# Performance work log

Measured on AMD Instinct MI355X. Metric: run time of the kernel, lower is better.

The kernel has to match this reference:

```python
import jax, jax.numpy as jnp
import numpy as np

D = 1024            # text/user embedding length
HID = 3 * D         # 2*text_D + user_D = MLP hidden width
OUT = 8             # output_shape (int)


def setup_inputs() -> dict:
    key = jax.random.key(0)
    ks = jax.random.split(key, 9)
    T, U = 256, 128
    s = 1.0 / np.sqrt(HID)
    return {
        "text_a": jax.random.normal(ks[0], (T, D), jnp.float32),
        "text_b": jax.random.normal(ks[1], (T, D), jnp.float32),
        "user_embeddings": jax.random.normal(ks[2], (U, D), jnp.float32),
        "W1": jax.random.uniform(ks[3], (HID, HID), jnp.float32, -s, s),
        "b1": jax.random.uniform(ks[4], (HID,), jnp.float32, -s, s),
        "W2": jax.random.uniform(ks[5], (HID, HID), jnp.float32, -s, s),
        "b2": jax.random.uniform(ks[6], (HID,), jnp.float32, -s, s),
        "W3": jax.random.uniform(ks[7], (OUT, HID), jnp.float32, -s, s),
        "b3": jax.random.uniform(ks[8], (OUT,), jnp.float32, -s, s),
    }


def reference(text_a, text_b, user_embeddings, W1, b1, W2, b2, W3, b3):
    # min/max over the set of text embedding tensors
    t_min = jnp.minimum(text_a, text_b)          # (T, D)
    t_max = jnp.maximum(text_a, text_b)          # (T, D)
    T, U = t_min.shape[0], user_embeddings.shape[0]
    # combined[t, u] = concat(t_min[t], t_max[t], user[u])  -> (T, U, 3D)
    text_part = jnp.broadcast_to(
        jnp.concatenate([t_min, t_max], axis=-1)[:, None, :], (T, U, 2 * D))
    user_part = jnp.broadcast_to(user_embeddings[None, :, :], (T, U, D))
    x = jnp.concatenate([text_part, user_part], axis=-1)  # (T, U, 3D)
    # 3-layer MLP (no activation, no dropout by default)
    x = jnp.einsum('tuh,oh->tuo', x, W1) + b1
    x = jnp.einsum('tuh,oh->tuo', x, W2) + b2
    x = jnp.einsum('tuh,oh->tuo', x, W3) + b3
    return x  # (T, U, OUT)
```

## Files before the change

### kernel.cpp

```cpp
#include <hip/hip_runtime.h>
#include <hip/hip_bf16.h>


#define HIDN 3072
#define DIM 1024
#define NOUT 8
#define NS 32
#define KPS 96
#define WK 24
#define GX 12
#define TDIM 256
#define UDIM 128

__device__ __forceinline__ float dot4(float4 a, float4 b) {
    return a.x * b.x + a.y * b.y + a.z * b.z + a.w * b.w;
}

__device__ __forceinline__ void bias_slice_fold(const float* As,
                                                const float* __restrict__ bvec,
                                                float* __restrict__ cp,
                                                int s, int tid) {
    const int o = tid >> 5, k5 = tid & 31;
    float acc = 0.f;
#pragma unroll
    for (int j = 0; j < KPS / 32; ++j)
        acc += As[o * KPS + k5 + 32 * j] * bvec[s * KPS + k5 + 32 * j];
#pragma unroll
    for (int off = 16; off; off >>= 1) acc += __shfl_down(acc, off, 32);
    if (k5 == 0) cp[s * NOUT + o] = acc;
}

__global__ __launch_bounds__(256) void gemm_partial(
    const float* __restrict__ A_rows, const float* __restrict__ part_in,
    const float* __restrict__ B, float* __restrict__ part_out,
    const float* __restrict__ bvec, float* __restrict__ cp, int mode) {
    const int s = blockIdx.y, gx = blockIdx.x;
    const int tid = threadIdx.x;
    const int lane = tid & 63, w = tid >> 6;

    __shared__ float As[NOUT * KPS];
    __shared__ float4 red[4 * NOUT * 64];

    if (mode == 0) {
        for (int i = tid; i < NOUT * KPS; i += 256)
            As[i] = A_rows[(i / KPS) * HIDN + s * KPS + (i % KPS)];
    } else {
        for (int j4 = tid; j4 < NOUT * KPS / 4; j4 += 256) {
            const int o = j4 / (KPS / 4), kk4 = j4 % (KPS / 4);
            const float4* pp = (const float4*)(part_in + (size_t)o * HIDN
                                               + s * KPS) + kk4;
            float4 a = make_float4(0.f, 0.f, 0.f, 0.f);
#pragma unroll 8
            for (int sp = 0; sp < NS; ++sp) {
                float4 v = pp[(size_t)sp * (NOUT * HIDN / 4)];
                a.x += v.x; a.y += v.y; a.z += v.z; a.w += v.w;
            }
            ((float4*)As)[j4] = a;
        }
    }
    __syncthreads();
    if (gx == 0) bias_slice_fold(As, bvec, cp, s, tid);

    const int h = gx * 256 + lane * 4;
    const int k0 = s * KPS + w * WK;
    const float4* Bp = (const float4*)(B + (size_t)k0 * HIDN) + (h >> 2);

    float4 bv[WK];
#pragma unroll
    for (int kk = 0; kk < WK; ++kk) bv[kk] = Bp[(size_t)kk * (HIDN / 4)];

    float4 acc[NOUT];
#pragma unroll
    for (int o = 0; o < NOUT; ++o) acc[o] = make_float4(0.f, 0.f, 0.f, 0.f);
#pragma unroll
    for (int kk = 0; kk < WK; ++kk) {
#pragma unroll
        for (int o = 0; o < NOUT; ++o) {
            float a = As[o * KPS + w * WK + kk];
            acc[o].x += a * bv[kk].x; acc[o].y += a * bv[kk].y;
            acc[o].z += a * bv[kk].z; acc[o].w += a * bv[kk].w;
        }
    }

#pragma unroll
    for (int o = 0; o < NOUT; ++o) red[(w * NOUT + o) * 64 + lane] = acc[o];
    __syncthreads();
#pragma unroll
    for (int j = 0; j < 2; ++j) {
        const int o = w * 2 + j;
        float4 v0 = red[(0 * NOUT + o) * 64 + lane];
        float4 v1 = red[(1 * NOUT + o) * 64 + lane];
        float4 v2 = red[(2 * NOUT + o) * 64 + lane];
        float4 v3 = red[(3 * NOUT + o) * 64 + lane];
        *(float4*)(part_out + ((size_t)s * NOUT + o) * HIDN + h) =
            make_float4(v0.x + v1.x + v2.x + v3.x, v0.y + v1.y + v2.y + v3.y,
                        v0.z + v1.z + v2.z + v3.z, v0.w + v1.w + v2.w + v3.w);
    }
}

__global__ __launch_bounds__(256) void reduce_M_c(const float* __restrict__ part,
                                                  const float* __restrict__ cp1,
                                                  const float* __restrict__ cp2,
                                                  const float* __restrict__ b3,
                                                  float* __restrict__ M,
                                                  float* __restrict__ c) {
    const int b = blockIdx.x, tid = threadIdx.x;
    if (b == 96) {
        if (tid < NOUT) {
            float acc = b3[tid];
            for (int s = 0; s < NS; ++s)
                acc += cp1[s * NOUT + tid] + cp2[s * NOUT + tid];
            c[tid] = acc;
        }
        return;
    }
    const int lane = tid & 63, w = tid >> 6;
    const int i4 = b * 64 + lane;
    const float4* p = (const float4*)part;
    float4 acc = make_float4(0.f, 0.f, 0.f, 0.f);
#pragma unroll
    for (int j = 0; j < NS / 4; ++j) {
        float4 v = p[(size_t)(w * (NS / 4) + j) * (NOUT * HIDN / 4) + i4];
        acc.x += v.x; acc.y += v.y; acc.z += v.z; acc.w += v.w;
    }
    __shared__ float4 red[4 * 64];
    red[w * 64 + lane] = acc;
    __syncthreads();
    if (w == 0) {
        float4 a0 = red[lane], a1 = red[64 + lane];
        float4 a2 = red[128 + lane], a3 = red[192 + lane];
        ((float4*)M)[i4] = make_float4(
            a0.x + a1.x + a2.x + a3.x, a0.y + a1.y + a2.y + a3.y,
            a0.z + a1.z + a2.z + a3.z, a0.w + a1.w + a2.w + a3.w);
    }
}

__global__ __launch_bounds__(256) void proj(const float* __restrict__ ta,
                                            const float* __restrict__ tb,
                                            const float* __restrict__ user,
                                            const float* __restrict__ M,
                                            float* __restrict__ P,
                                            float* __restrict__ Q) {
    const int tid = threadIdx.x;
    const int bid = blockIdx.x;
    const int lane = tid & 63, w = tid >> 6;
    const int d = tid * 4;
    float acc[NOUT];

    if (bid < TDIM) {
        const int t = bid;
        float4 a = *(const float4*)(ta + t * DIM + d);
        float4 b = *(const float4*)(tb + t * DIM + d);
        float4 mn = make_float4(fminf(a.x, b.x), fminf(a.y, b.y),
                                fminf(a.z, b.z), fminf(a.w, b.w));
        float4 mx = make_float4(fmaxf(a.x, b.x), fmaxf(a.y, b.y),
                                fmaxf(a.z, b.z), fmaxf(a.w, b.w));
#pragma unroll
        for (int o = 0; o < NOUT; ++o) {
            float4 ml = *(const float4*)(M + o * HIDN + d);
            float4 mh = *(const float4*)(M + o * HIDN + DIM + d);
            acc[o] = dot4(ml, mn) + dot4(mh, mx);
        }
    } else {
        const int u = bid - TDIM;
        float4 x = *(const float4*)(user + u * DIM + d);
#pragma unroll
        for (int o = 0; o < NOUT; ++o) {
            float4 m = *(const float4*)(M + o * HIDN + 2 * DIM + d);
            acc[o] = dot4(m, x);
        }
    }

#pragma unroll
    for (int o = 0; o < NOUT; ++o) {
#pragma unroll
        for (int off = 32; off > 0; off >>= 1)
            acc[o] += __shfl_down(acc[o], off, 64);
    }
    __shared__ float red[4][NOUT];
    if (lane == 0) {
#pragma unroll
        for (int o = 0; o < NOUT; ++o) red[w][o] = acc[o];
    }
    __syncthreads();
    float* dst = (bid < TDIM) ? (P + bid * NOUT) : (Q + (bid - TDIM) * NOUT);
    if (tid < NOUT) dst[tid] = red[0][tid] + red[1][tid] + red[2][tid] + red[3][tid];
}

__global__ __launch_bounds__(256) void combine_out(const float* __restrict__ P,
                                                   const float* __restrict__ Q,
                                                   const float* __restrict__ c,
                                                   float4* __restrict__ out) {
    const int idx = blockIdx.x * 256 + threadIdx.x;
    const int t = idx >> 7, u = idx & (UDIM - 1);
    const float4* Pp = (const float4*)(P) + t * 2;
    const float4* Qp = (const float4*)(Q) + u * 2;
    const float4* Cp = (const float4*)(c);
    float4 p0 = Pp[0], p1 = Pp[1];
    float4 q0 = Qp[0], q1 = Qp[1];
    float4 c0 = Cp[0], c1 = Cp[1];
    out[idx * 2]     = make_float4(p0.x + q0.x + c0.x, p0.y + q0.y + c0.y,
                                   p0.z + q0.z + c0.z, p0.w + q0.w + c0.w);
    out[idx * 2 + 1] = make_float4(p1.x + q1.x + c1.x, p1.y + q1.y + c1.y,
                                   p1.z + q1.z + c1.z, p1.w + q1.w + c1.w);
}

extern "C" void kernel_launch(void* const* d_in, const int* in_sizes, int n_in,
                              void* d_out, int out_size, void* d_ws, size_t ws_size,
                              hipStream_t stream) {
    const float* text_a = (const float*)d_in[0];
    const float* text_b = (const float*)d_in[1];
    const float* user   = (const float*)d_in[2];
    const float* W1 = (const float*)d_in[3];
    const float* b1 = (const float*)d_in[4];
    const float* W2 = (const float*)d_in[5];
    const float* b2 = (const float*)d_in[6];
    const float* W3 = (const float*)d_in[7];
    const float* b3 = (const float*)d_in[8];

    float* ws = (float*)d_ws;
    float* part1 = ws;
    float* part2 = part1 + (size_t)NS * NOUT * HIDN;
    float* M  = part2 + (size_t)NS * NOUT * HIDN;
    float* c  = M + NOUT * HIDN;
    float* cp1 = c + NOUT;
    float* cp2 = cp1 + NS * NOUT;
    float* P  = cp2 + NS * NOUT;
    float* Q  = P + TDIM * NOUT;

    gemm_partial<<<dim3(GX, NS), 256, 0, stream>>>(W3, nullptr, W2, part1,
                                                   b2, cp2, 0);
    gemm_partial<<<dim3(GX, NS), 256, 0, stream>>>(nullptr, part1, W1, part2,
                                                   b1, cp1, 1);
    reduce_M_c<<<97, 256, 0, stream>>>(part2, cp1, cp2, b3, M, c);
    proj<<<TDIM + UDIM, 256, 0, stream>>>(text_a, text_b, user, M, P, Q);
    combine_out<<<(TDIM * UDIM) / 256, 256, 0, stream>>>(P, Q, c, (float4*)d_out);
}
```

Measured before the change: 34.01 us.

## Fuse partial reduction, user projection and output combine into fewer kernels

Replaces the reduce_M_c, proj and combine_out kernels with two kernels. mid_kernel reduces the split-K partials into the text half of M and also computes per-slice user projections directly from the partials. out_kernel computes the text projections, sums the user slices and the bias constant, and writes the final output. This removes one launch and the intermediate P/Q round trips. In exchange, each output block redundantly re-reads Qpart and the bias partials, and mid_kernel runs on only 24 blocks.

```diff
diff --git a/kernel.cpp b/kernel.cpp
--- a/kernel.cpp
+++ b/kernel.cpp
@@ -15,6 +15,9 @@
 __device__ __forceinline__ float dot4(float4 a, float4 b) {
     return a.x * b.x + a.y * b.y + a.z * b.z + a.w * b.w;
 }
+__device__ __forceinline__ float4 add4(float4 a, float4 b) {
+    return make_float4(a.x + b.x, a.y + b.y, a.z + b.z, a.w + b.w);
+}
 
 __device__ __forceinline__ void bias_slice_fold(const float* As,
                                                 const float* __restrict__ bvec,
@@ -51,10 +54,8 @@
                                                + s * KPS) + kk4;
             float4 a = make_float4(0.f, 0.f, 0.f, 0.f);
 #pragma unroll 8
-            for (int sp = 0; sp < NS; ++sp) {
-                float4 v = pp[(size_t)sp * (NOUT * HIDN / 4)];
-                a.x += v.x; a.y += v.y; a.z += v.z; a.w += v.w;
-            }
+            for (int sp = 0; sp < NS; ++sp)
+                a = add4(a, pp[(size_t)sp * (NOUT * HIDN / 4)]);
             ((float4*)As)[j4] = a;
         }
     }
@@ -88,89 +89,79 @@
 #pragma unroll
     for (int j = 0; j < 2; ++j) {
         const int o = w * 2 + j;
-        float4 v0 = red[(0 * NOUT + o) * 64 + lane];
-        float4 v1 = red[(1 * NOUT + o) * 64 + lane];
-        float4 v2 = red[(2 * NOUT + o) * 64 + lane];
-        float4 v3 = red[(3 * NOUT + o) * 64 + lane];
-        *(float4*)(part_out + ((size_t)s * NOUT + o) * HIDN + h) =
-            make_float4(v0.x + v1.x + v2.x + v3.x, v0.y + v1.y + v2.y + v3.y,
-                        v0.z + v1.z + v2.z + v3.z, v0.w + v1.w + v2.w + v3.w);
-    }
-}
-
-__global__ __launch_bounds__(256) void reduce_M_c(const float* __restrict__ part,
-                                                  const float* __restrict__ cp1,
-                                                  const float* __restrict__ cp2,
-                                                  const float* __restrict__ b3,
-                                                  float* __restrict__ M,
-                                                  float* __restrict__ c) {
+        float4 r = add4(add4(red[(0 * NOUT + o) * 64 + lane],
+                             red[(1 * NOUT + o) * 64 + lane]),
+                        add4(red[(2 * NOUT + o) * 64 + lane],
+                             red[(3 * NOUT + o) * 64 + lane]));
+        *(float4*)(part_out + ((size_t)s * NOUT + o) * HIDN + h) = r;
+    }
+}
+
+__global__ __launch_bounds__(256) void mid_kernel(const float* __restrict__ part2,
+                                                  const float* __restrict__ user,
+                                                  float* __restrict__ Mt,
+                                                  float* __restrict__ Qpart) {
     const int b = blockIdx.x, tid = threadIdx.x;
-    if (b == 96) {
-        if (tid < NOUT) {
-            float acc = b3[tid];
-            for (int s = 0; s < NS; ++s)
-                acc += cp1[s * NOUT + tid] + cp2[s * NOUT + tid];
-            c[tid] = acc;
-        }
+    const float4* p4 = (const float4*)part2;
+
+    if (b < 16) {
+        const int i4 = b * 256 + tid;
+        const int o = i4 >> 9, j4 = i4 & 511;
+        float4 a = make_float4(0.f, 0.f, 0.f, 0.f);
+#pragma unroll 8
+        for (int s = 0; s < NS; ++s)
+            a = add4(a, p4[((size_t)s * NOUT + o) * (HIDN / 4) + j4]);
+        ((float4*)Mt)[o * 512 + j4] = a;
         return;
     }
+
+    const int dg = b - 16;
+    __shared__ float4 Mu4[NOUT * 32];
+    {
+        const int o = tid >> 5, j4 = tid & 31;
+        float4 a = make_float4(0.f, 0.f, 0.f, 0.f);
+#pragma unroll 8
+        for (int s = 0; s < NS; ++s)
+            a = add4(a, p4[((size_t)s * NOUT + o) * (HIDN / 4) + 512 + dg * 32 + j4]);
+        Mu4[o * 32 + j4] = a;
+    }
+    __syncthreads();
+
+    const int u = tid >> 1, o0 = (tid & 1) * 4;
+    const float4* uv = (const float4*)(user) + u * (DIM / 4) + dg * 32;
+    float q[4] = {0.f, 0.f, 0.f, 0.f};
+    for (int j = 0; j < 32; ++j) {
+        float4 x = uv[j];
+#pragma unroll
+        for (int oo = 0; oo < 4; ++oo)
+            q[oo] += dot4(Mu4[(o0 + oo) * 32 + j], x);
+    }
+    *(float4*)(Qpart + ((size_t)dg * UDIM + u) * NOUT + o0) =
+        make_float4(q[0], q[1], q[2], q[3]);
+}
+
+__global__ __launch_bounds__(256) void out_kernel(
+    const float* __restrict__ ta, const float* __restrict__ tb,
+    const float* __restrict__ Mt, const float* __restrict__ Qpart,
+    const float* __restrict__ cp1, const float* __restrict__ cp2,
+    const float* __restrict__ b3, float4* __restrict__ out) {
+    const int t = blockIdx.x, tid = threadIdx.x;
     const int lane = tid & 63, w = tid >> 6;
-    const int i4 = b * 64 + lane;
-    const float4* p = (const float4*)part;
-    float4 acc = make_float4(0.f, 0.f, 0.f, 0.f);
-#pragma unroll
-    for (int j = 0; j < NS / 4; ++j) {
-        float4 v = p[(size_t)(w * (NS / 4) + j) * (NOUT * HIDN / 4) + i4];
-        acc.x += v.x; acc.y += v.y; acc.z += v.z; acc.w += v.w;
-    }
-    __shared__ float4 red[4 * 64];
-    red[w * 64 + lane] = acc;
-    __syncthreads();
-    if (w == 0) {
-        float4 a0 = red[lane], a1 = red[64 + lane];
-        float4 a2 = red[128 + lane], a3 = red[192 + lane];
-        ((float4*)M)[i4] = make_float4(
-            a0.x + a1.x + a2.x + a3.x, a0.y + a1.y + a2.y + a3.y,
-            a0.z + a1.z + a2.z + a3.z, a0.w + a1.w + a2.w + a3.w);
-    }
-}
-
-__global__ __launch_bounds__(256) void proj(const float* __restrict__ ta,
-                                            const float* __restrict__ tb,
-                                            const float* __restrict__ user,
-                                            const float* __restrict__ M,
-                                            float* __restrict__ P,
-                                            float* __restrict__ Q) {
-    const int tid = threadIdx.x;
-    const int bid = blockIdx.x;
-    const int lane = tid & 63, w = tid >> 6;
-    const int d = tid * 4;
+
+    const float4* Mt4 = (const float4*)Mt;
+    float4 a = ((const float4*)ta)[t * (DIM / 4) + tid];
+    float4 b = ((const float4*)tb)[t * (DIM / 4) + tid];
+    float4 mn = make_float4(fminf(a.x, b.x), fminf(a.y, b.y),
+                            fminf(a.z, b.z), fminf(a.w, b.w));
+    float4 mx = make_float4(fmaxf(a.x, b.x), fmaxf(a.y, b.y),
+                            fmaxf(a.z, b.z), fmaxf(a.w, b.w));
     float acc[NOUT];
-
-    if (bid < TDIM) {
-        const int t = bid;
-        float4 a = *(const float4*)(ta + t * DIM + d);
-        float4 b = *(const float4*)(tb + t * DIM + d);
-        float4 mn = make_float4(fminf(a.x, b.x), fminf(a.y, b.y),
-                                fminf(a.z, b.z), fminf(a.w, b.w));
-        float4 mx = make_float4(fmaxf(a.x, b.x), fmaxf(a.y, b.y),
-                                fmaxf(a.z, b.z), fmaxf(a.w, b.w));
-#pragma unroll
-        for (int o = 0; o < NOUT; ++o) {
-            float4 ml = *(const float4*)(M + o * HIDN + d);
-            float4 mh = *(const float4*)(M + o * HIDN + DIM + d);
-            acc[o] = dot4(ml, mn) + dot4(mh, mx);
-        }
-    } else {
-        const int u = bid - TDIM;
-        float4 x = *(const float4*)(user + u * DIM + d);
-#pragma unroll
-        for (int o = 0; o < NOUT; ++o) {
-            float4 m = *(const float4*)(M + o * HIDN + 2 * DIM + d);
-            acc[o] = dot4(m, x);
-        }
-    }
-
+#pragma unroll
+    for (int o = 0; o < NOUT; ++o) {
+        float4 ml = Mt4[o * 512 + tid];
+        float4 mh = Mt4[o * 512 + 256 + tid];
+        acc[o] = dot4(ml, mn) + dot4(mh, mx);
+    }
 #pragma unroll
     for (int o = 0; o < NOUT; ++o) {
 #pragma unroll
@@ -178,31 +169,36 @@
             acc[o] += __shfl_down(acc[o], off, 64);
     }
     __shared__ float red[4][NOUT];
+    __shared__ float c8[NOUT];
     if (lane == 0) {
 #pragma unroll
         for (int o = 0; o < NOUT; ++o) red[w][o] = acc[o];
     }
-    __syncthreads();
-    float* dst = (bid < TDIM) ? (P + bid * NOUT) : (Q + (bid - TDIM) * NOUT);
-    if (tid < NOUT) dst[tid] = red[0][tid] + red[1][tid] + red[2][tid] + red[3][tid];
-}
-
-__global__ __launch_bounds__(256) void combine_out(const float* __restrict__ P,
-                                                   const float* __restrict__ Q,
-                                                   const float* __restrict__ c,
-                                                   float4* __restrict__ out) {
-    const int idx = blockIdx.x * 256 + threadIdx.x;
-    const int t = idx >> 7, u = idx & (UDIM - 1);
-    const float4* Pp = (const float4*)(P) + t * 2;
-    const float4* Qp = (const float4*)(Q) + u * 2;
-    const float4* Cp = (const float4*)(c);
-    float4 p0 = Pp[0], p1 = Pp[1];
-    float4 q0 = Qp[0], q1 = Qp[1];
-    float4 c0 = Cp[0], c1 = Cp[1];
-    out[idx * 2]     = make_float4(p0.x + q0.x + c0.x, p0.y + q0.y + c0.y,
-                                   p0.z + q0.z + c0.z, p0.w + q0.w + c0.w);
-    out[idx * 2 + 1] = make_float4(p1.x + q1.x + c1.x, p1.y + q1.y + c1.y,
-                                   p1.z + q1.z + c1.z, p1.w + q1.w + c1.w);
+
+    const int u = tid >> 1, half = tid & 1;
+    const float4* Qp4 = (const float4*)Qpart;
+    float4 q = make_float4(0.f, 0.f, 0.f, 0.f);
+#pragma unroll
+    for (int dg = 0; dg < 8; ++dg)
+        q = add4(q, Qp4[((size_t)dg * UDIM + u) * 2 + half]);
+
+    if (tid < NOUT) {
+        float cc = b3[tid];
+#pragma unroll 8
+        for (int s = 0; s < NS; ++s)
+            cc += cp1[s * NOUT + tid] + cp2[s * NOUT + tid];
+        c8[tid] = cc;
+    }
+    __syncthreads();
+
+    const int o0 = half * 4;
+    float4 pv = make_float4(
+        red[0][o0 + 0] + red[1][o0 + 0] + red[2][o0 + 0] + red[3][o0 + 0],
+        red[0][o0 + 1] + red[1][o0 + 1] + red[2][o0 + 1] + red[3][o0 + 1],
+        red[0][o0 + 2] + red[1][o0 + 2] + red[2][o0 + 2] + red[3][o0 + 2],
+        red[0][o0 + 3] + red[1][o0 + 3] + red[2][o0 + 3] + red[3][o0 + 3]);
+    float4 cv = make_float4(c8[o0], c8[o0 + 1], c8[o0 + 2], c8[o0 + 3]);
+    out[(size_t)t * 256 + tid] = add4(add4(pv, q), cv);
 }
 
 extern "C" void kernel_launch(void* const* d_in, const int* in_sizes, int n_in,
@@ -221,18 +217,16 @@
     float* ws = (float*)d_ws;
     float* part1 = ws;
     float* part2 = part1 + (size_t)NS * NOUT * HIDN;
-    float* M  = part2 + (size_t)NS * NOUT * HIDN;
-    float* c  = M + NOUT * HIDN;
-    float* cp1 = c + NOUT;
-    float* cp2 = cp1 + NS * NOUT;
-    float* P  = cp2 + NS * NOUT;
-    float* Q  = P + TDIM * NOUT;
+    float* Mt    = part2 + (size_t)NS * NOUT * HIDN;
+    float* Qpart = Mt + NOUT * 2048;
+    float* cp1   = Qpart + 8 * UDIM * NOUT;
+    float* cp2   = cp1 + NS * NOUT;
 
     gemm_partial<<<dim3(GX, NS), 256, 0, stream>>>(W3, nullptr, W2, part1,
                                                    b2, cp2, 0);
     gemm_partial<<<dim3(GX, NS), 256, 0, stream>>>(nullptr, part1, W1, part2,
                                                    b1, cp1, 1);
-    reduce_M_c<<<97, 256, 0, stream>>>(part2, cp1, cp2, b3, M, c);
-    proj<<<TDIM + UDIM, 256, 0, stream>>>(text_a, text_b, user, M, P, Q);
-    combine_out<<<(TDIM * UDIM) / 256, 256, 0, stream>>>(P, Q, c, (float4*)d_out);
-}
+    mid_kernel<<<24, 256, 0, stream>>>(part2, user, Mt, Qpart);
+    out_kernel<<<TDIM, 256, 0, stream>>>(text_a, text_b, Mt, Qpart,
+                                         cp1, cp2, b3, (float4*)d_out);
+}
```

After: 36.93 us. 8.6% more time.
